# Kernel optimization log

Measured on AMD Instinct MI355X. Metric: run time of the kernel, lower is better.

Reference implementation:

```python
import jax, jax.numpy as jnp
import numpy as np

BETA1T = 20.0
BETA0 = 1e-4
T = 1000

def setup_inputs() -> dict:
    key = jax.random.key(0)
    # timesteps uniformly in [0, T]
    t = jax.random.uniform(key, (16777216,), dtype=jnp.float32) * T
    return {"t": t}

def reference(t):
    # beta(s) = beta0 * (1 - (s-1)/(T-1)) + (beta1T/T) * ((s-1)/(T-1)),  s = 1..T
    s = jnp.arange(1, T + 1, dtype=t.dtype)
    frac = (s - 1.0) / (T - 1.0)
    beta = BETA0 * (1.0 - frac) + (BETA1T / T) * frac
    # cumulative sum of log alpha_s; prepend 0 so index 0 -> empty product = 1
    clog = jnp.concatenate([jnp.zeros((1,), dtype=t.dtype),
                            jnp.cumsum(jnp.log1p(-beta))])  # [T+1]
    idx = jnp.clip(jnp.round(t).astype(jnp.int32), 0, T)
    return jnp.exp(clog[idx])
```

## Files before the change

### kernel.cpp

```cpp
#include <hip/hip_runtime.h>

#define T_STEPS 1000
#define BETA0   1e-4f
#define BETA1T  20.0f

__global__ void ddpm_build_table(float* __restrict__ table) {
    __shared__ float partial[256];
    const int tid = threadIdx.x;

    float vals[4];
    float local = 0.0f;
    #pragma unroll
    for (int j = 0; j < 4; ++j) {
        int k = tid * 4 + j;
        float v = 0.0f;
        if (k < T_STEPS) {
            float frac = (float)k / (float)(T_STEPS - 1);
            float beta = BETA0 * (1.0f - frac) + (BETA1T / (float)T_STEPS) * frac;
            v = log1pf(-beta);
        }
        local += v;
        vals[j] = local;
    }
    partial[tid] = local;
    __syncthreads();

    #pragma unroll
    for (int off = 1; off < 256; off <<= 1) {
        float add = (tid >= off) ? partial[tid - off] : 0.0f;
        __syncthreads();
        partial[tid] += add;
        __syncthreads();
    }
    float prefix = (tid > 0) ? partial[tid - 1] : 0.0f;

    if (tid == 0) table[0] = 1.0f;
    #pragma unroll
    for (int j = 0; j < 4; ++j) {
        int k = tid * 4 + j;
        if (k < T_STEPS) table[k + 1] = expf(prefix + vals[j]);
    }
}

__global__ __launch_bounds__(256)
void ddpm_gather(const float* __restrict__ t,
                 float* __restrict__ out,
                 const float* __restrict__ table,
                 int n) {
    __shared__ float lut[T_STEPS + 1];
    for (int i = threadIdx.x; i < T_STEPS + 1; i += blockDim.x)
        lut[i] = table[i];
    __syncthreads();

    const int gid = blockIdx.x * blockDim.x + threadIdx.x;
    const int n4  = n >> 2;

    if (gid < n4) {
        const float4* __restrict__ t4 = (const float4*)t;
        float4*       __restrict__ o4 = (float4*)out;
        float4 v = t4[gid];
        int i0 = (int)rintf(v.x); i0 = min(max(i0, 0), T_STEPS);
        int i1 = (int)rintf(v.y); i1 = min(max(i1, 0), T_STEPS);
        int i2 = (int)rintf(v.z); i2 = min(max(i2, 0), T_STEPS);
        int i3 = (int)rintf(v.w); i3 = min(max(i3, 0), T_STEPS);
        float4 r;
        r.x = lut[i0];
        r.y = lut[i1];
        r.z = lut[i2];
        r.w = lut[i3];
        o4[gid] = r;
    }

    int tail = n - (n4 << 2);
    if (gid < tail) {
        int k = (n4 << 2) + gid;
        int i = (int)rintf(t[k]); i = min(max(i, 0), T_STEPS);
        out[k] = lut[i];
    }
}

extern "C" void kernel_launch(void* const* d_in, const int* in_sizes, int n_in,
                              void* d_out, int out_size, void* d_ws, size_t ws_size,
                              hipStream_t stream) {
    const float* t = (const float*)d_in[0];
    float* out     = (float*)d_out;
    float* table   = (float*)d_ws;
    const int n    = in_sizes[0];

    ddpm_build_table<<<1, 256, 0, stream>>>(table);

    int n4     = n >> 2;
    int blocks = (n4 + 255) / 256;
    if (blocks < 1) blocks = 1;
    ddpm_gather<<<blocks, 256, 0, stream>>>(t, out, table, n);
}
```

Measured before the change: 117.5 us.

## Replace table build and LDS gather with closed-form polynomial cumulative log

Computes the cumulative log-alpha directly as a cubic polynomial in the rounded timestep, derived from a truncated log1p series summed in closed form, then applies exp2. This removes the single-block table-building kernel, the workspace table, and the per-block shared-memory LUT load and barrier. The trade-off is a small approximation error from truncating the series and float rounding of coefficients.

```diff
diff --git a/kernel.cpp b/kernel.cpp
--- a/kernel.cpp
+++ b/kernel.cpp
@@ -1,81 +1,57 @@
 #include <hip/hip_runtime.h>
 
-#define T_STEPS 1000
-#define BETA0   1e-4f
-#define BETA1T  20.0f
+namespace {
+constexpr double a_  = 1e-4;
+constexpr double d_  = (20.0 / 1000.0 - 1e-4) / 999.0;
 
-__global__ void ddpm_build_table(float* __restrict__ table) {
-    __shared__ float partial[256];
-    const int tid = threadIdx.x;
+constexpr double A1d = (a_ - d_ / 2.0)
+                     + (a_ * a_ - a_ * d_ + d_ * d_ / 6.0) / 2.0
+                     + (a_ * a_ * a_ - 1.5 * a_ * a_ * d_ + 0.5 * a_ * d_ * d_) / 3.0;
+constexpr double A2d = d_ / 2.0
+                     + (a_ * d_ - d_ * d_ / 2.0) / 2.0
+                     + (1.5 * a_ * a_ * d_ - 1.5 * a_ * d_ * d_ + 0.25 * d_ * d_ * d_) / 3.0;
+constexpr double A3d = d_ * d_ / 6.0
+                     + (a_ * d_ * d_ - 0.5 * d_ * d_ * d_) / 3.0;
+constexpr double A4d = d_ * d_ * d_ / 12.0;
 
-    float vals[4];
-    float local = 0.0f;
-    #pragma unroll
-    for (int j = 0; j < 4; ++j) {
-        int k = tid * 4 + j;
-        float v = 0.0f;
-        if (k < T_STEPS) {
-            float frac = (float)k / (float)(T_STEPS - 1);
-            float beta = BETA0 * (1.0f - frac) + (BETA1T / (float)T_STEPS) * frac;
-            v = log1pf(-beta);
-        }
-        local += v;
-        vals[j] = local;
-    }
-    partial[tid] = local;
-    __syncthreads();
+constexpr float A1 = (float)A1d;
+constexpr float A2 = (float)A2d;
+constexpr float A3 = (float)A3d;
+constexpr float A4 = (float)A4d;
+constexpr float LOG2E = 1.4426950408889634f;
+}
 
-    #pragma unroll
-    for (int off = 1; off < 256; off <<= 1) {
-        float add = (tid >= off) ? partial[tid - off] : 0.0f;
-        __syncthreads();
-        partial[tid] += add;
-        __syncthreads();
-    }
-    float prefix = (tid > 0) ? partial[tid - 1] : 0.0f;
-
-    if (tid == 0) table[0] = 1.0f;
-    #pragma unroll
-    for (int j = 0; j < 4; ++j) {
-        int k = tid * 4 + j;
-        if (k < T_STEPS) table[k + 1] = expf(prefix + vals[j]);
-    }
+__device__ __forceinline__ float alpha_bar(float v) {
+    float k = __builtin_rintf(v);
+    k = fminf(fmaxf(k, 0.0f), 1000.0f);
+    float p = fmaf(k, A4, A3);
+    p = fmaf(k, p, A2);
+    p = fmaf(k, p, A1);
+    float clog = -k * p;
+    return exp2f(clog * LOG2E);
 }
 
 __global__ __launch_bounds__(256)
-void ddpm_gather(const float* __restrict__ t,
-                 float* __restrict__ out,
-                 const float* __restrict__ table,
-                 int n) {
-    __shared__ float lut[T_STEPS + 1];
-    for (int i = threadIdx.x; i < T_STEPS + 1; i += blockDim.x)
-        lut[i] = table[i];
-    __syncthreads();
-
+void ddpm_alpha_bar(const float* __restrict__ t,
+                    float* __restrict__ out,
+                    int n) {
     const int gid = blockIdx.x * blockDim.x + threadIdx.x;
     const int n4  = n >> 2;
 
     if (gid < n4) {
-        const float4* __restrict__ t4 = (const float4*)t;
-        float4*       __restrict__ o4 = (float4*)out;
-        float4 v = t4[gid];
-        int i0 = (int)rintf(v.x); i0 = min(max(i0, 0), T_STEPS);
-        int i1 = (int)rintf(v.y); i1 = min(max(i1, 0), T_STEPS);
-        int i2 = (int)rintf(v.z); i2 = min(max(i2, 0), T_STEPS);
-        int i3 = (int)rintf(v.w); i3 = min(max(i3, 0), T_STEPS);
+        float4 v = ((const float4*)t)[gid];
         float4 r;
-        r.x = lut[i0];
-        r.y = lut[i1];
-        r.z = lut[i2];
-        r.w = lut[i3];
-        o4[gid] = r;
+        r.x = alpha_bar(v.x);
+        r.y = alpha_bar(v.y);
+        r.z = alpha_bar(v.z);
+        r.w = alpha_bar(v.w);
+        ((float4*)out)[gid] = r;
     }
 
     int tail = n - (n4 << 2);
     if (gid < tail) {
         int k = (n4 << 2) + gid;
-        int i = (int)rintf(t[k]); i = min(max(i, 0), T_STEPS);
-        out[k] = lut[i];
+        out[k] = alpha_bar(t[k]);
     }
 }
 
@@ -84,13 +60,10 @@
                               hipStream_t stream) {
     const float* t = (const float*)d_in[0];
     float* out     = (float*)d_out;
-    float* table   = (float*)d_ws;
     const int n    = in_sizes[0];
 
-    ddpm_build_table<<<1, 256, 0, stream>>>(table);
-
-    int n4     = n >> 2;
+    int n4     = (n + 3) >> 2;
     int blocks = (n4 + 255) / 256;
     if (blocks < 1) blocks = 1;
-    ddpm_gather<<<blocks, 256, 0, stream>>>(t, out, table, n);
+    ddpm_alpha_bar<<<blocks, 256, 0, stream>>>(t, out, n);
 }
```

Result: faster. 109.0 us (-7.3%).
